# Kernel tuning notes

Hardware: AMD Instinct MI355X
Metric: run time of the kernel (lower is better)

Reference implementation:

```python
import jax, jax.numpy as jnp
import numpy as np
import math

B, N, DIM, H = 4, 2048, 1024, 16
DH = DIM // H

def setup_inputs() -> dict:
    key = jax.random.key(0)
    ks = jax.random.split(key, 7)
    return {
        "x": jax.random.normal(ks[0], (B, N, DIM), dtype=jnp.float32),
        "qkv_w": jax.random.normal(ks[1], (3 * DIM, DIM), dtype=jnp.float32) * 0.02,
        "qkv_b": jax.random.normal(ks[2], (3 * DIM,), dtype=jnp.float32) * 0.02,
        "proj_w": jax.random.normal(ks[3], (DIM, DIM), dtype=jnp.float32) * 0.02,
        "proj_b": jax.random.normal(ks[4], (DIM,), dtype=jnp.float32) * 0.02,
        "temperature": jnp.ones((1,), dtype=jnp.float32) * 0.1,
        "eps": jax.random.normal(ks[5], (B, H, N, DH), dtype=jnp.float32),
    }

def reference(x, qkv_w, qkv_b, proj_w, proj_b, temperature, eps):
    b, n, dim = x.shape
    qkv = x @ qkv_w.T + qkv_b
    qkv = qkv.reshape(b, n, 3, H, DH).transpose(2, 0, 3, 1, 4)
    q, k, v = qkv[0], qkv[1], qkv[2]
    # quantum fluctuation: additive gaussian noise on q, scaled by sigmoid(temperature)
    q = q + eps * jax.nn.sigmoid(temperature)
    scale = 1.0 / math.sqrt(DH)
    attn = jnp.einsum("bhqd,bhkd->bhqk", q, k) * scale  # [B,H,N,N]
    attn = jax.nn.softmax(attn, axis=-1)
    out = jnp.einsum("bhqk,bhkd->bhqd", attn, v)  # [B,H,N,DH]
    out = out.transpose(0, 2, 1, 3).reshape(b, n, dim)
    return out @ proj_w.T + proj_b
```

## Files before the change

### kernel.cpp

```cpp
#include <hip/hip_runtime.h>
#include <math.h>

#define B_   4
#define N_   2048
#define DIM_ 1024
#define H_   16
#define DH_  64
#define M_   (B_ * N_)
#define QKV_ELEMS ((size_t)B_ * H_ * N_ * DH_)

typedef __attribute__((ext_vector_type(8))) short short8;
typedef __attribute__((ext_vector_type(4))) float floatx4;

static __device__ inline unsigned short f2bf(float f) {
    union { float f; unsigned u; } v; v.f = f;
    unsigned r = (v.u + 0x7fffu + ((v.u >> 16) & 1u)) >> 16;
    return (unsigned short)r;
}

static __device__ inline void async_copy16(const void* g, void* l) {
    __builtin_amdgcn_global_load_lds(
        (const __attribute__((address_space(1))) unsigned int*)g,
        (__attribute__((address_space(3))) unsigned int*)l, 16, 0, 0);
}

__global__ __launch_bounds__(256) void f32_to_bf16_kernel(
    const float* __restrict__ src, unsigned short* __restrict__ dst, int n8)
{
    int i = blockIdx.x * 256 + threadIdx.x;
    if (i >= n8) return;
    float4 a = ((const float4*)src)[i * 2];
    float4 b = ((const float4*)src)[i * 2 + 1];
    short8 o;
    o[0] = f2bf(a.x); o[1] = f2bf(a.y); o[2] = f2bf(a.z); o[3] = f2bf(a.w);
    o[4] = f2bf(b.x); o[5] = f2bf(b.y); o[6] = f2bf(b.z); o[7] = f2bf(b.w);
    *(short8*)(dst + (size_t)i * 8) = o;
}

#define GEMM_BODY(Aptr, Bptr, K)                                               \
    __shared__ unsigned short As[128 * 32];                                    \
    __shared__ unsigned short Bs[128 * 32];                                    \
    const int tid  = threadIdx.x;                                              \
    const int lane = tid & 63;                                                 \
    const int wv   = tid >> 6;                                                 \
    const int l15  = lane & 15, quad = lane >> 4;                              \
    const int wrow = (wv >> 1) * 64, wcol = (wv & 1) * 64;                     \
    const int m0 = blockIdx.y * 128, n0 = blockIdx.x * 128;                    \
    const int lrow = lane >> 2;                                                \
    const int lkc  = (lane & 3) * 8;                                           \
    const unsigned short* ga0 = Aptr + (size_t)(m0 + wv * 32 + lrow) * K + lkc;\
    const unsigned short* ga1 = ga0 + (size_t)16 * K;                          \
    const unsigned short* gb0 = Bptr + (size_t)(n0 + wv * 32 + lrow) * K + lkc;\
    const unsigned short* gb1 = gb0 + (size_t)16 * K;                          \
    unsigned short* lA0 = &As[wv * 1024];                                      \
    unsigned short* lA1 = lA0 + 512;                                           \
    unsigned short* lB0 = &Bs[wv * 1024];                                      \
    unsigned short* lB1 = lB0 + 512;                                           \
    floatx4 acc[4][4] = {};                                                    \
    for (int k0 = 0; k0 < K; k0 += 32) {                                       \
        __syncthreads();                                                       \
        async_copy16(ga0 + k0, lA0);                                           \
        async_copy16(ga1 + k0, lA1);                                           \
        async_copy16(gb0 + k0, lB0);                                           \
        async_copy16(gb1 + k0, lB1);                                           \
        __syncthreads();                                                       \
        short8 af[4], bf[4];                                                   \
        _Pragma("unroll")                                                      \
        for (int mt = 0; mt < 4; ++mt)                                         \
            af[mt] = *(const short8*)&As[(wrow + mt * 16 + l15) * 32 + quad * 8];\
        _Pragma("unroll")                                                      \
        for (int nt = 0; nt < 4; ++nt)                                         \
            bf[nt] = *(const short8*)&Bs[(wcol + nt * 16 + l15) * 32 + quad * 8];\
        _Pragma("unroll")                                                      \
        for (int mt = 0; mt < 4; ++mt)                                         \
            _Pragma("unroll")                                                  \
            for (int nt = 0; nt < 4; ++nt)                                     \
                acc[mt][nt] = __builtin_amdgcn_mfma_f32_16x16x32_bf16(         \
                    af[mt], bf[nt], acc[mt][nt], 0, 0, 0);                     \
    }

__global__ __launch_bounds__(256) void gemm_qkv_bf16(
    const unsigned short* __restrict__ A, const unsigned short* __restrict__ Bm,
    const float* __restrict__ bias, const float* __restrict__ eps,
    const float* __restrict__ temp,
    unsigned short* __restrict__ qb, unsigned short* __restrict__ kb,
    unsigned short* __restrict__ vb)
{
    GEMM_BODY(A, Bm, 1024)

    const float sig = 1.0f / (1.0f + __expf(-temp[0]));
    const float qscale = 0.125f * 1.44269504f;
#pragma unroll
    for (int mt = 0; mt < 4; ++mt) {
#pragma unroll
        for (int r = 0; r < 4; ++r) {
            const int m  = m0 + wrow + mt * 16 + quad * 4 + r;
            const int b  = m >> 11;
            const int nn = m & 2047;
#pragma unroll
            for (int nt = 0; nt < 4; ++nt) {
                const int n = n0 + wcol + nt * 16 + l15;
                float val = acc[mt][nt][r] + bias[n];
                const int which = n >> 10;
                const int d  = n & 1023;
                const int h  = d >> 6;
                const int dd = d & 63;
                const size_t bh = (size_t)(b * H_ + h);
                if (which == 0) {
                    const size_t idx = (bh * N_ + nn) * DH_ + dd;
                    qb[idx] = f2bf((val + eps[idx] * sig) * qscale);
                } else if (which == 1) {
                    kb[(bh * N_ + nn) * DH_ + dd] = f2bf(val);
                } else {
                    vb[(bh * DH_ + dd) * N_ + nn] = f2bf(val);
                }
            }
        }
    }
}

__global__ __launch_bounds__(256) void gemm_proj_bf16(
    const unsigned short* __restrict__ A, const unsigned short* __restrict__ Bm,
    const float* __restrict__ bias, float* __restrict__ out)
{
    GEMM_BODY(A, Bm, 1024)

#pragma unroll
    for (int mt = 0; mt < 4; ++mt) {
#pragma unroll
        for (int r = 0; r < 4; ++r) {
            const int m = m0 + wrow + mt * 16 + quad * 4 + r;
#pragma unroll
            for (int nt = 0; nt < 4; ++nt) {
                const int n = n0 + wcol + nt * 16 + l15;
                out[(size_t)m * 1024 + n] = acc[mt][nt][r] + bias[n];
            }
        }
    }
}

__global__ __launch_bounds__(256) void attn_kernel(
    const unsigned short* __restrict__ qb, const unsigned short* __restrict__ kb,
    const unsigned short* __restrict__ vt, unsigned short* __restrict__ attn_out)
{
    __shared__ unsigned short Ks[64 * 72];
    __shared__ unsigned short Vs[64 * 72];
    __shared__ unsigned short Ps[64 * 72];

    const int tid  = threadIdx.x;
    const int lane = tid & 63;
    const int wv   = tid >> 6;
    const int l15  = lane & 15;
    const int quad = lane >> 4;

    const int bh = blockIdx.y;
    const int b  = bh >> 4, h = bh & 15;
    const int q0 = blockIdx.x * 64;
    const int qr = q0 + wv * 16;

    const unsigned short* qp = qb + ((size_t)bh * N_ + qr + l15) * DH_;
    const short8 qf0 = *(const short8*)(qp + quad * 8);
    const short8 qf1 = *(const short8*)(qp + 32 + quad * 8);

    floatx4 o[4] = {};
    float l_acc[4] = {0.f, 0.f, 0.f, 0.f};

    const unsigned short* kb_bh = kb + (size_t)bh * N_ * DH_;
    const unsigned short* vt_bh = vt + (size_t)bh * DH_ * N_;

    for (int kt = 0; kt < 32; ++kt) {
        const unsigned short* kbase = kb_bh + (size_t)kt * 64 * DH_;
        const unsigned short* vbase = vt_bh + kt * 64;

        __syncthreads();
#pragma unroll
        for (int c = tid; c < 512; c += 256) {
            int r = c >> 3, off = (c & 7) << 3;
            *(short8*)&Ks[r * 72 + off] = *(const short8*)(kbase + r * 64 + off);
            *(short8*)&Vs[r * 72 + off] = *(const short8*)(vbase + (size_t)r * N_ + off);
        }
        __syncthreads();

        floatx4 s[4];
#pragma unroll
        for (int nt = 0; nt < 4; ++nt) {
            const unsigned short* krow = &Ks[(nt * 16 + l15) * 72];
            short8 kf0 = *(const short8*)(krow + quad * 8);
            short8 kf1 = *(const short8*)(krow + 32 + quad * 8);
            floatx4 c = {};
            c = __builtin_amdgcn_mfma_f32_16x16x32_bf16(qf0, kf0, c, 0, 0, 0);
            c = __builtin_amdgcn_mfma_f32_16x16x32_bf16(qf1, kf1, c, 0, 0, 0);
            s[nt] = c;
        }

#pragma unroll
        for (int nt = 0; nt < 4; ++nt)
#pragma unroll
            for (int r = 0; r < 4; ++r)
                s[nt][r] = __builtin_amdgcn_exp2f(s[nt][r]);
#pragma unroll
        for (int r = 0; r < 4; ++r)
            l_acc[r] += (s[0][r] + s[1][r]) + (s[2][r] + s[3][r]);

#pragma unroll
        for (int nt = 0; nt < 4; ++nt)
#pragma unroll
            for (int r = 0; r < 4; ++r) {
                unsigned u = (__float_as_uint(s[nt][r]) + 0x8000u) >> 16;
                Ps[(wv * 16 + quad * 4 + r) * 72 + nt * 16 + l15] = (unsigned short)u;
            }

        const unsigned short* prow = &Ps[(wv * 16 + l15) * 72];
        short8 pf0 = *(const short8*)(prow + quad * 8);
        short8 pf1 = *(const short8*)(prow + 32 + quad * 8);

#pragma unroll
        for (int dt = 0; dt < 4; ++dt) {
            const unsigned short* vrow = &Vs[(dt * 16 + l15) * 72];
            short8 vf0 = *(const short8*)(vrow + quad * 8);
            short8 vf1 = *(const short8*)(vrow + 32 + quad * 8);
            o[dt] = __builtin_amdgcn_mfma_f32_16x16x32_bf16(pf0, vf0, o[dt], 0, 0, 0);
            o[dt] = __builtin_amdgcn_mfma_f32_16x16x32_bf16(pf1, vf1, o[dt], 0, 0, 0);
        }
    }

    float inv[4];
#pragma unroll
    for (int r = 0; r < 4; ++r) {
        float l = l_acc[r];
#pragma unroll
        for (int off = 1; off < 16; off <<= 1)
            l += __shfl_xor(l, off, 64);
        inv[r] = 1.0f / l;
    }

#pragma unroll
    for (int dt = 0; dt < 4; ++dt) {
#pragma unroll
        for (int r = 0; r < 4; ++r) {
            int m = qr + quad * 4 + r;
            attn_out[((size_t)b * N_ + m) * DIM_ + h * DH_ + dt * 16 + l15] =
                f2bf(o[dt][r] * inv[r]);
        }
    }
}

extern "C" void kernel_launch(void* const* d_in, const int* in_sizes, int n_in,
                              void* d_out, int out_size, void* d_ws, size_t ws_size,
                              hipStream_t stream) {
    const float* x      = (const float*)d_in[0];
    const float* qkv_w  = (const float*)d_in[1];
    const float* qkv_b  = (const float*)d_in[2];
    const float* proj_w = (const float*)d_in[3];
    const float* proj_b = (const float*)d_in[4];
    const float* temp   = (const float*)d_in[5];
    const float* eps    = (const float*)d_in[6];
    float* out = (float*)d_out;

    unsigned short* qb   = (unsigned short*)d_ws;
    unsigned short* kb   = qb + QKV_ELEMS;
    unsigned short* vb   = kb + QKV_ELEMS;
    unsigned short* xb   = vb + QKV_ELEMS;
    unsigned short* wqb  = xb + QKV_ELEMS;
    unsigned short* pwb  = wqb + (size_t)3 * DIM_ * DIM_;
    unsigned short* attn = pwb + (size_t)DIM_ * DIM_;

    dim3 blk(256);
    f32_to_bf16_kernel<<<dim3(8388608 / 8 / 256), blk, 0, stream>>>(x, xb, 8388608 / 8);
    f32_to_bf16_kernel<<<dim3(3145728 / 8 / 256), blk, 0, stream>>>(qkv_w, wqb, 3145728 / 8);
    f32_to_bf16_kernel<<<dim3(1048576 / 8 / 256), blk, 0, stream>>>(proj_w, pwb, 1048576 / 8);

    gemm_qkv_bf16<<<dim3(24, 64), blk, 0, stream>>>(xb, wqb, qkv_b, eps, temp,
                                                    qb, kb, vb);
    attn_kernel<<<dim3(32, 64), blk, 0, stream>>>(qb, kb, vb, attn);
    gemm_proj_bf16<<<dim3(8, 64), blk, 0, stream>>>(attn, pwb, proj_b, out);
}
```

Before: 407.8 us.

## Restructure attention to single-wave blocks reading K/V directly from global

The attention kernel now runs one 64-lane wave per block, and each wave handles 32 query rows as two 16-row MFMA tiles. K and V fragments are loaded straight from global memory into registers instead of being staged through shared memory. This removes the block-wide barriers, and each K/V fragment is reused across both query tiles. The P tile in LDS gets an XOR swizzle to cut bank conflicts. In exchange, K/V loads now depend on L2/L1 caching with no LDS reuse across waves, and the global V loads are strided by N.

```diff
diff --git a/kernel.cpp b/kernel.cpp
--- a/kernel.cpp
+++ b/kernel.cpp
@@ -139,108 +139,101 @@
     }
 }
 
-__global__ __launch_bounds__(256) void attn_kernel(
+__global__ __launch_bounds__(64) void attn_kernel(
     const unsigned short* __restrict__ qb, const unsigned short* __restrict__ kb,
     const unsigned short* __restrict__ vt, unsigned short* __restrict__ attn_out)
 {
-    __shared__ unsigned short Ks[64 * 72];
-    __shared__ unsigned short Vs[64 * 72];
-    __shared__ unsigned short Ps[64 * 72];
-
-    const int tid  = threadIdx.x;
-    const int lane = tid & 63;
-    const int wv   = tid >> 6;
+    __shared__ unsigned short Ps[32 * 72];
+
+    const int lane = threadIdx.x;
     const int l15  = lane & 15;
     const int quad = lane >> 4;
 
     const int bh = blockIdx.y;
     const int b  = bh >> 4, h = bh & 15;
-    const int q0 = blockIdx.x * 64;
-    const int qr = q0 + wv * 16;
-
-    const unsigned short* qp = qb + ((size_t)bh * N_ + qr + l15) * DH_;
-    const short8 qf0 = *(const short8*)(qp + quad * 8);
-    const short8 qf1 = *(const short8*)(qp + 32 + quad * 8);
-
-    floatx4 o[4] = {};
-    float l_acc[4] = {0.f, 0.f, 0.f, 0.f};
+    const int qr = blockIdx.x * 32;
+
+    short8 qf[2][2];
+#pragma unroll
+    for (int mt = 0; mt < 2; ++mt) {
+        const unsigned short* qp = qb + ((size_t)bh * N_ + qr + mt * 16 + l15) * DH_;
+        qf[mt][0] = *(const short8*)(qp + quad * 8);
+        qf[mt][1] = *(const short8*)(qp + 32 + quad * 8);
+    }
+
+    floatx4 o[2][4] = {};
+    float l_acc[2][4] = {};
 
     const unsigned short* kb_bh = kb + (size_t)bh * N_ * DH_;
     const unsigned short* vt_bh = vt + (size_t)bh * DH_ * N_;
 
     for (int kt = 0; kt < 32; ++kt) {
-        const unsigned short* kbase = kb_bh + (size_t)kt * 64 * DH_;
-        const unsigned short* vbase = vt_bh + kt * 64;
-
-        __syncthreads();
-#pragma unroll
-        for (int c = tid; c < 512; c += 256) {
-            int r = c >> 3, off = (c & 7) << 3;
-            *(short8*)&Ks[r * 72 + off] = *(const short8*)(kbase + r * 64 + off);
-            *(short8*)&Vs[r * 72 + off] = *(const short8*)(vbase + (size_t)r * N_ + off);
-        }
-        __syncthreads();
-
-        floatx4 s[4];
+        const unsigned short* kk = kb_bh + (size_t)kt * 64 * DH_;
+
 #pragma unroll
         for (int nt = 0; nt < 4; ++nt) {
-            const unsigned short* krow = &Ks[(nt * 16 + l15) * 72];
+            const unsigned short* krow = kk + (size_t)(nt * 16 + l15) * DH_;
             short8 kf0 = *(const short8*)(krow + quad * 8);
             short8 kf1 = *(const short8*)(krow + 32 + quad * 8);
-            floatx4 c = {};
-            c = __builtin_amdgcn_mfma_f32_16x16x32_bf16(qf0, kf0, c, 0, 0, 0);
-            c = __builtin_amdgcn_mfma_f32_16x16x32_bf16(qf1, kf1, c, 0, 0, 0);
-            s[nt] = c;
-        }
-
-#pragma unroll
-        for (int nt = 0; nt < 4; ++nt)
-#pragma unroll
-            for (int r = 0; r < 4; ++r)
-                s[nt][r] = __builtin_amdgcn_exp2f(s[nt][r]);
-#pragma unroll
-        for (int r = 0; r < 4; ++r)
-            l_acc[r] += (s[0][r] + s[1][r]) + (s[2][r] + s[3][r]);
-
-#pragma unroll
-        for (int nt = 0; nt < 4; ++nt)
-#pragma unroll
-            for (int r = 0; r < 4; ++r) {
-                unsigned u = (__float_as_uint(s[nt][r]) + 0x8000u) >> 16;
-                Ps[(wv * 16 + quad * 4 + r) * 72 + nt * 16 + l15] = (unsigned short)u;
-            }
-
-        const unsigned short* prow = &Ps[(wv * 16 + l15) * 72];
-        short8 pf0 = *(const short8*)(prow + quad * 8);
-        short8 pf1 = *(const short8*)(prow + 32 + quad * 8);
-
+            const int col = nt * 16 + l15;
+#pragma unroll
+            for (int mt = 0; mt < 2; ++mt) {
+                floatx4 c = {};
+                c = __builtin_amdgcn_mfma_f32_16x16x32_bf16(qf[mt][0], kf0, c, 0, 0, 0);
+                c = __builtin_amdgcn_mfma_f32_16x16x32_bf16(qf[mt][1], kf1, c, 0, 0, 0);
+#pragma unroll
+                for (int r = 0; r < 4; ++r) {
+                    float p = __builtin_amdgcn_exp2f(c[r]);
+                    l_acc[mt][r] += p;
+                    const int row = mt * 16 + quad * 4 + r;
+                    unsigned u = (__float_as_uint(p) + 0x8000u) >> 16;
+                    Ps[row * 72 + (col ^ ((row & 12) << 2))] = (unsigned short)u;
+                }
+            }
+        }
+
+        short8 pf[2][2];
+#pragma unroll
+        for (int mt = 0; mt < 2; ++mt) {
+            const int row = mt * 16 + l15;
+            const int swz = (row & 12) << 2;
+            pf[mt][0] = *(const short8*)&Ps[row * 72 + ((quad * 8) ^ swz)];
+            pf[mt][1] = *(const short8*)&Ps[row * 72 + ((32 + quad * 8) ^ swz)];
+        }
+
+        const unsigned short* vv = vt_bh + kt * 64;
 #pragma unroll
         for (int dt = 0; dt < 4; ++dt) {
-            const unsigned short* vrow = &Vs[(dt * 16 + l15) * 72];
+            const unsigned short* vrow = vv + (size_t)(dt * 16 + l15) * N_;
             short8 vf0 = *(const short8*)(vrow + quad * 8);
             short8 vf1 = *(const short8*)(vrow + 32 + quad * 8);
-            o[dt] = __builtin_amdgcn_mfma_f32_16x16x32_bf16(pf0, vf0, o[dt], 0, 0, 0);
-            o[dt] = __builtin_amdgcn_mfma_f32_16x16x32_bf16(pf1, vf1, o[dt], 0, 0, 0);
-        }
-    }
-
-    float inv[4];
-#pragma unroll
-    for (int r = 0; r < 4; ++r) {
-        float l = l_acc[r];
-#pragma unroll
-        for (int off = 1; off < 16; off <<= 1)
-            l += __shfl_xor(l, off, 64);
-        inv[r] = 1.0f / l;
-    }
-
-#pragma unroll
-    for (int dt = 0; dt < 4; ++dt) {
+#pragma unroll
+            for (int mt = 0; mt < 2; ++mt) {
+                o[mt][dt] = __builtin_amdgcn_mfma_f32_16x16x32_bf16(pf[mt][0], vf0, o[mt][dt], 0, 0, 0);
+                o[mt][dt] = __builtin_amdgcn_mfma_f32_16x16x32_bf16(pf[mt][1], vf1, o[mt][dt], 0, 0, 0);
+            }
+        }
+    }
+
+#pragma unroll
+    for (int mt = 0; mt < 2; ++mt) {
+        float inv[4];
 #pragma unroll
         for (int r = 0; r < 4; ++r) {
-            int m = qr + quad * 4 + r;
-            attn_out[((size_t)b * N_ + m) * DIM_ + h * DH_ + dt * 16 + l15] =
-                f2bf(o[dt][r] * inv[r]);
+            float l = l_acc[mt][r];
+#pragma unroll
+            for (int off = 1; off < 16; off <<= 1)
+                l += __shfl_xor(l, off, 64);
+            inv[r] = 1.0f / l;
+        }
+#pragma unroll
+        for (int dt = 0; dt < 4; ++dt) {
+#pragma unroll
+            for (int r = 0; r < 4; ++r) {
+                const int m = qr + mt * 16 + quad * 4 + r;
+                attn_out[((size_t)b * N_ + m) * DIM_ + h * DH_ + dt * 16 + l15] =
+                    f2bf(o[mt][dt][r] * inv[r]);
+            }
         }
     }
 }
@@ -272,6 +265,6 @@
 
     gemm_qkv_bf16<<<dim3(24, 64), blk, 0, stream>>>(xb, wqb, qkv_b, eps, temp,
                                                     qb, kb, vb);
-    attn_kernel<<<dim3(32, 64), blk, 0, stream>>>(qb, kb, vb, attn);
+    attn_kernel<<<dim3(64, 64), dim3(64), 0, stream>>>(qb, kb, vb, attn);
     gemm_proj_bf16<<<dim3(8, 64), blk, 0, stream>>>(attn, pwb, proj_b, out);
 }
```

Measured after the change: 506.0 us. +24.1%, slower.
